# Kernel tuning notes

Measured on AMD Instinct MI355X. Metric: run time of the kernel, lower is better.

## Reference

```python
import jax, jax.numpy as jnp
import numpy as np
from jax import lax

D_STATE = 16
D_CONV = 4
D_MODEL = 1024
D_INNER = 2048
DT_RANK = 64
SEQLEN = 2048
BATCH = 2


def setup_inputs() -> dict:
    key = jax.random.key(0)
    ks = jax.random.split(key, 8)
    hidden_states = jax.random.normal(ks[0], (SEQLEN, BATCH, D_MODEL), jnp.float32)
    W_in = jax.random.normal(ks[1], (2 * D_INNER, D_MODEL), jnp.float32) * (D_MODEL ** -0.5)
    conv_w = jax.random.normal(ks[2], (D_INNER, D_CONV), jnp.float32) * (D_CONV ** -0.5)
    conv_b = jnp.zeros((D_INNER,), jnp.float32)
    W_x = jax.random.normal(ks[3], (DT_RANK + 2 * D_STATE, D_INNER), jnp.float32) * (D_INNER ** -0.5)
    dt_init_std = DT_RANK ** -0.5
    W_dt = jax.random.uniform(ks[4], (D_INNER, DT_RANK), jnp.float32, -dt_init_std, dt_init_std)
    # dt bias init: inverse-softplus of dt ~ LogUniform(1e-3, 1e-1)
    dt = jnp.exp(jax.random.uniform(ks[5], (D_INNER,), jnp.float32) * (np.log(0.1) - np.log(0.001)) + np.log(0.001))
    dt = jnp.clip(dt, 1e-4, None)
    dt_bias = dt + jnp.log(-jnp.expm1(-dt))
    A_log = jnp.log(jnp.tile(jnp.arange(1, D_STATE + 1, dtype=jnp.float32)[None, :], (D_INNER, 1)))
    Dp = jnp.ones((D_INNER,), jnp.float32)
    W_out = jax.random.normal(ks[6], (D_MODEL, D_INNER), jnp.float32) * (D_INNER ** -0.5)
    return {"hidden_states": hidden_states, "W_in": W_in, "conv_w": conv_w, "conv_b": conv_b,
            "W_x": W_x, "W_dt": W_dt, "dt_bias": dt_bias, "A_log": A_log, "D": Dp, "W_out": W_out}


def _mamba_forward(hidden_states, W_in, conv_w, conv_b, W_x, W_dt, dt_bias, A_log, D, W_out):
    L, B, _ = hidden_states.shape
    d_inner, d_state = A_log.shape
    dt_rank = W_dt.shape[1]
    # in_proj: [L,B,D] -> [L,B,2*d_inner] -> [B,2*d_inner,L]
    xz = jnp.einsum('lbd,ed->lbe', hidden_states, W_in)
    xz = jnp.transpose(xz, (1, 2, 0))
    x, z = jnp.split(xz, 2, axis=1)  # each [B,d_inner,L]
    # causal depthwise conv1d + silu
    x = lax.conv_general_dilated(x, conv_w[:, None, :], (1,), [(D_CONV - 1, 0)],
                                 dimension_numbers=('NCH', 'OIH', 'NCH'),
                                 feature_group_count=d_inner)
    x = jax.nn.silu(x + conv_b[None, :, None])  # [B,d_inner,L]
    # x_proj over (b l) tokens
    x_bl = jnp.transpose(x, (0, 2, 1)).reshape(B * L, d_inner)  # (b l) d
    x_dbl = x_bl @ W_x.T  # [(b l), dt_rank + 2*d_state]
    dt_lr, Bm, Cm = jnp.split(x_dbl, [dt_rank, dt_rank + d_state], axis=-1)
    dt = (W_dt @ dt_lr.T).reshape(d_inner, B, L).transpose(1, 0, 2)  # [B,d_inner,L]
    Bm = Bm.reshape(B, L, d_state)  # [B,L,n]
    Cm = Cm.reshape(B, L, d_state)
    # selective scan (delta_softplus=True, delta_bias=dt_bias)
    A = -jnp.exp(A_log)  # [d_inner, n]
    delta = jax.nn.softplus(dt + dt_bias[None, :, None])  # [B,d,L]
    delta_t = jnp.transpose(delta, (2, 0, 1))  # [L,B,d]
    u_t = jnp.transpose(x, (2, 0, 1))          # [L,B,d]
    B_t = jnp.transpose(Bm, (1, 0, 2))         # [L,B,n]
    C_t = jnp.transpose(Cm, (1, 0, 2))         # [L,B,n]

    def step(state, inp):
        d_i, u_i, b_i, c_i = inp
        dA = jnp.exp(d_i[:, :, None] * A[None])           # [B,d,n]
        dBu = (d_i * u_i)[:, :, None] * b_i[:, None, :]   # [B,d,n]
        state = state * dA + dBu
        y = jnp.einsum('bdn,bn->bd', state, c_i)
        return state, y

    init = jnp.zeros((B, d_inner, d_state), delta.dtype)
    _, ys = lax.scan(step, init, (delta_t, u_t, B_t, C_t))  # ys [L,B,d]
    y = jnp.transpose(ys, (1, 0, 2))                         # [B,L,d]
    y = y + jnp.transpose(x, (0, 2, 1)) * D[None, None, :]
    y = y * jax.nn.silu(jnp.transpose(z, (0, 2, 1)))
    out = y @ W_out.T  # [B,L,d_model]
    return jnp.transpose(out, (1, 0, 2))  # [L,B,d_model]


def reference(hidden_states, W_in, conv_w, conv_b, W_x, W_dt, dt_bias, A_log, D, W_out):
    return _mamba_forward(hidden_states, W_in, conv_w, conv_b, W_x, W_dt, dt_bias, A_log, D, W_out)
```

## Files before the change

### kernel.cpp

```cpp
#include <hip/hip_runtime.h>
#include <hip/hip_bf16.h>


#define L_SEQ 2048
#define N_B   2
#define D_M   1024
#define D_I   2048
#define D_ST  16
#define R_DT  64
#define CHNK  32
#define CT    64
#define KS    8
#define DUS   68

using bf16 = __hip_bfloat16;
typedef unsigned short u16;
typedef unsigned int u32;
typedef u16 u16x8 __attribute__((ext_vector_type(8)));
typedef __bf16 bf16x8 __attribute__((ext_vector_type(8)));
typedef float f32x4 __attribute__((ext_vector_type(4)));

__device__ __forceinline__ float b2f(u16 u) {
    union { u32 i; float f; } x;
    x.i = ((u32)u) << 16;
    return x.f;
}
__device__ __forceinline__ u16 f2b(float f) {
    union { bf16 h; u16 s; } x;
    x.h = __float2bfloat16(f);
    return x.s;
}

__device__ __forceinline__ void load4(const float* p, float* o) {
    const float4 v = *(const float4*)p;
    o[0] = v.x; o[1] = v.y; o[2] = v.z; o[3] = v.w;
}
__device__ __forceinline__ void load4(const bf16* p, float* o) {
    const ushort4 v = *(const ushort4*)(const void*)p;
    o[0] = b2f(v.x); o[1] = b2f(v.y); o[2] = b2f(v.z); o[3] = b2f(v.w);
}

__device__ __forceinline__ float softplus_f(float x) {
    return (x > 20.f) ? x : log1pf(__expf(x));
}
__device__ __forceinline__ float silu_f(float x) {
    return x / (1.f + __expf(-x));
}

__device__ __forceinline__ void gl_lds16(const u16* g, u16* l) {
    __builtin_amdgcn_global_load_lds(
        (const __attribute__((address_space(1))) void*)g,
        (__attribute__((address_space(3))) void*)l, 16, 0, 0);
}

template <int EPI>
__global__ __launch_bounds__(256) void bgemm(
    const u16* __restrict__ A, int lda,
    const u16* __restrict__ Wb, int ldb, int K,
    u16* __restrict__ bd, float* __restrict__ fout,
    const float* __restrict__ bias)
{
    __shared__ u16 As[128 * 32];
    __shared__ u16 Bs[64 * 32];

    const int tid = threadIdx.x;
    const int m0 = blockIdx.x * 128;
    const int n0 = blockIdx.y * 64;
    const int w  = tid >> 6;
    const int ln = tid & 63;

    const int sr0 = (w << 4) + (ln >> 2);
    const int sr1 = sr0 + 64;
    const int sx  = ln & 3;
    const int qa0 = (sx - (sr0 >> 1)) & 3;
    const int qa1 = (sx - (sr1 >> 1)) & 3;

    const u16* ga0 = A  + (size_t)(m0 + sr0) * lda + qa0 * 8;
    const u16* ga1 = A  + (size_t)(m0 + sr1) * lda + qa1 * 8;
    const u16* gb0 = Wb + (size_t)(n0 + sr0) * ldb + qa0 * 8;
    u16* la0 = As + ((w << 4) + 0) * 32;
    u16* la1 = As + ((w << 4) + 64) * 32;
    u16* lb0 = Bs + (w << 4) * 32;

    const int wr = (w >> 1) << 6;
    const int wc = (w & 1) << 5;
    const int lm = ln & 15;
    const int qf = ln >> 4;
    int aoff[4], boff[2];
#pragma unroll
    for (int i = 0; i < 4; ++i) {
        const int ra = wr + i * 16 + lm;
        aoff[i] = ra * 32 + (((qf + (ra >> 1)) & 3) << 3);
    }
#pragma unroll
    for (int j = 0; j < 2; ++j) {
        const int rb = wc + j * 16 + lm;
        boff[j] = rb * 32 + (((qf + (rb >> 1)) & 3) << 3);
    }

    f32x4 acc[4][2] = {};

    for (int k0 = 0; k0 < K; k0 += 32) {
        if (k0) __syncthreads();
        gl_lds16(ga0 + k0, la0);
        gl_lds16(ga1 + k0, la1);
        gl_lds16(gb0 + k0, lb0);
        __syncthreads();

        bf16x8 af[4], bfr[2];
#pragma unroll
        for (int i = 0; i < 4; ++i) af[i] = *(const bf16x8*)&As[aoff[i]];
#pragma unroll
        for (int j = 0; j < 2; ++j) bfr[j] = *(const bf16x8*)&Bs[boff[j]];
#pragma unroll
        for (int i = 0; i < 4; ++i)
#pragma unroll
            for (int j = 0; j < 2; ++j)
                acc[i][j] = __builtin_amdgcn_mfma_f32_16x16x32_bf16(
                    af[i], bfr[j], acc[i][j], 0, 0, 0);
    }

    const int qr = (ln >> 4) << 2;
    float bv[2];
    if (EPI == 2) {
#pragma unroll
        for (int j = 0; j < 2; ++j) bv[j] = bias[n0 + wc + j * 16 + lm];
    }
#pragma unroll
    for (int i = 0; i < 4; ++i) {
#pragma unroll
        for (int reg = 0; reg < 4; ++reg) {
            const int rg = m0 + wr + i * 16 + qr + reg;
            if (EPI == 0) {
                const int bb = rg & (N_B - 1);
                const int l = rg >> 1;
                const size_t t = (size_t)bb * L_SEQ + l;
#pragma unroll
                for (int j = 0; j < 2; ++j)
                    bd[t * D_I + n0 + wc + j * 16 + lm] = f2b(acc[i][j][reg]);
            } else if (EPI == 1) {
                const int bb = rg >> 11;
                const int l = rg & (L_SEQ - 1);
                const size_t o = ((size_t)l * N_B + bb) * D_M;
#pragma unroll
                for (int j = 0; j < 2; ++j)
                    fout[o + n0 + wc + j * 16 + lm] = acc[i][j][reg];
            } else if (EPI == 2) {
                const size_t t = (size_t)rg;
#pragma unroll
                for (int j = 0; j < 2; ++j)
                    bd[t * D_I + n0 + wc + j * 16 + lm] =
                        f2b(softplus_f(acc[i][j][reg] + bv[j]));
            } else {
                const int bb = rg & (N_B - 1);
                const int l = rg >> 1;
                const size_t t = (size_t)bb * L_SEQ + l;
#pragma unroll
                for (int j = 0; j < 2; ++j) {
                    u16* p = &bd[t * D_I + n0 + wc + j * 16 + lm];
                    *p = f2b(b2f(*p) * silu_f(acc[i][j][reg]));
                }
            }
        }
    }
}

__global__ __launch_bounds__(256) void xproj_k(
    const u16* __restrict__ u, const u16* __restrict__ Wxb,
    float* __restrict__ Part)
{
    __shared__ u16 As[64 * 32];
    __shared__ u16 Bs[96 * 264];

    const int tid = threadIdx.x;
    const int m0 = blockIdx.x * 64;
    const int kc = blockIdx.y;
    const int kbase = kc * 256;

    for (int e = tid; e < 96 * 32; e += 256) {
        const int row = e >> 5, kq = e & 31;
        const u16x8 v = *(const u16x8*)(Wxb + (size_t)row * D_I + kbase + kq * 8);
        *(u16x8*)&Bs[row * 264 + kq * 8] = v;
    }

    const int w  = tid >> 6;
    const int ln = tid & 63;
    const int sr = (w << 4) + (ln >> 2);
    const int sx = ln & 3;
    const int qa = (sx - (sr >> 1)) & 3;
    const u16* ga = u + (size_t)(m0 + sr) * D_I + kbase + qa * 8;
    u16* la = As + (w << 9);

    const int lm = ln & 15;
    const int qf = ln >> 4;
    const int ra = (w << 4) + lm;
    const int aoff = ra * 32 + (((qf + (ra >> 1)) & 3) << 3);

    f32x4 acc[6] = {};

    for (int it = 0; it < 8; ++it) {
        if (it) __syncthreads();
        gl_lds16(ga + it * 32, la);
        __syncthreads();

        const bf16x8 af = *(const bf16x8*)&As[aoff];
#pragma unroll
        for (int j = 0; j < 6; ++j) {
            const bf16x8 bfv = *(const bf16x8*)&Bs[(j * 16 + lm) * 264 + it * 32 + qf * 8];
            acc[j] = __builtin_amdgcn_mfma_f32_16x16x32_bf16(af, bfv, acc[j], 0, 0, 0);
        }
    }

    const int qr = (ln >> 4) << 2;
#pragma unroll
    for (int j = 0; j < 6; ++j) {
#pragma unroll
        for (int reg = 0; reg < 4; ++reg) {
            const int t = m0 + (w << 4) + qr + reg;
            Part[((size_t)kc * (N_B * L_SEQ) + t) * 96 + j * 16 + lm] = acc[j][reg];
        }
    }
}

__global__ __launch_bounds__(256) void xreduce(
    const float* __restrict__ Part, u16* __restrict__ dtlr,
    float* __restrict__ Bm, float* __restrict__ Cm)
{
    const int e = blockIdx.x * 256 + threadIdx.x;
    const int t = e / 96, c = e - t * 96;
    float s = 0.f;
#pragma unroll
    for (int kc = 0; kc < KS; ++kc)
        s += Part[(size_t)kc * (N_B * L_SEQ * 96) + e];
    if (c < 64)      dtlr[t * 64 + c] = f2b(s);
    else if (c < 80) Bm[t * 16 + (c - 64)] = s;
    else             Cm[t * 16 + (c - 80)] = s;
}

__global__ __launch_bounds__(256) void cvt_k(const float* __restrict__ s,
                                             u16* __restrict__ d)
{
    const size_t i = ((size_t)blockIdx.x * 256 + threadIdx.x) * 8;
    const float4 a = *(const float4*)(s + i);
    const float4 b = *(const float4*)(s + i + 4);
    u16 t[8] = {f2b(a.x), f2b(a.y), f2b(a.z), f2b(a.w),
                f2b(b.x), f2b(b.y), f2b(b.z), f2b(b.w)};
    *(u16x8*)(d + i) = *(const u16x8*)t;
}

__global__ __launch_bounds__(256) void conv_k(
    const bf16* __restrict__ x, const float* __restrict__ cw,
    const float* __restrict__ cb, bf16* __restrict__ xc)
{
    const int t = blockIdx.x;
    const int l = t & (L_SEQ - 1);
#pragma unroll
    for (int it = 0; it < 2; ++it) {
        const int d = ((int)threadIdx.x + it * 256) << 2;
        float w[4][4], bias[4], acc[4];
#pragma unroll
        for (int dd = 0; dd < 4; ++dd)
            load4(cw + (size_t)(d + dd) * 4, w[dd]);
        load4(cb + d, bias);
#pragma unroll
        for (int dd = 0; dd < 4; ++dd) acc[dd] = bias[dd];
#pragma unroll
        for (int j = 0; j < 4; ++j) {
            const int ll = l - 3 + j;
            if (ll >= 0) {
                float xv[4];
                load4(x + (size_t)(t - 3 + j) * D_I + d, xv);
#pragma unroll
                for (int dd = 0; dd < 4; ++dd)
                    acc[dd] = fmaf(xv[dd], w[dd][j], acc[dd]);
            }
        }
        const ushort4 v = make_ushort4(f2b(silu_f(acc[0])), f2b(silu_f(acc[1])),
                                       f2b(silu_f(acc[2])), f2b(silu_f(acc[3])));
        *(ushort4*)(void*)(xc + (size_t)t * D_I + d) = v;
    }
}

template <int PHASE>
__global__ __launch_bounds__(256) void scan_chunk(
    bf16* __restrict__ dy, const bf16* __restrict__ u,
    const float* __restrict__ Bm, const float* __restrict__ Cm,
    const float* __restrict__ Alog, const float* __restrict__ Dp,
    float* __restrict__ Pc, float* __restrict__ Qc,
    const float* __restrict__ Sin)
{
    __shared__ u32 duS[(CT / 2) * DUS];
    __shared__ float Bs[CT][D_ST];
    __shared__ float Cs[(PHASE == 1) ? CT : 1][D_ST];

    const int tid = threadIdx.x;
    const int d0 = blockIdx.x * 64;
    const int b  = blockIdx.y;
    const int c  = blockIdx.z;
    const int row0 = b * L_SEQ + c * CT;

    const int sl = tid >> 3;
    const int sg = tid & 7;

    u32 wB[8];
    {
        const size_t goA = (size_t)(row0 + sl) * D_I + d0 + sg * 8;
        const size_t goB = goA + (size_t)(CT / 2) * D_I;
        const u16x8 dA8 = *(const u16x8*)((const u16*)dy + goA);
        const u16x8 uA8 = *(const u16x8*)((const u16*)u + goA);
        const u16x8 dB8 = *(const u16x8*)((const u16*)dy + goB);
        const u16x8 uB8 = *(const u16x8*)((const u16*)u + goB);
        u32 wA[8];
#pragma unroll
        for (int j = 0; j < 8; ++j) {
            wA[j] = (u32)dA8[j] | ((u32)uA8[j] << 16);
            wB[j] = (u32)dB8[j] | ((u32)uB8[j] << 16);
        }
        *(uint4*)&duS[sl * DUS + sg * 8]     = make_uint4(wA[0], wA[1], wA[2], wA[3]);
        *(uint4*)&duS[sl * DUS + sg * 8 + 4] = make_uint4(wA[4], wA[5], wA[6], wA[7]);
    }
    {
        const float4* src = (const float4*)(Bm + (size_t)row0 * D_ST);
        float4* dst = (float4*)Bs;
        for (int e = tid; e < CT * D_ST / 4; e += 256) dst[e] = src[e];
        if (PHASE == 1) {
            const float4* s2 = (const float4*)(Cm + (size_t)row0 * D_ST);
            float4* d2 = (float4*)Cs;
            for (int e = tid; e < CT * D_ST / 4; e += 256) d2[e] = s2[e];
        }
    }
    __syncthreads();

    const int dl = tid >> 2;
    const int d  = d0 + dl;
    const int ns = tid & 3;
    const size_t pqbase = (((size_t)b * CHNK + c) * D_I + d) * D_ST + ns * 4;

    float Av[4];
    {
        const float4 a4 = *(const float4*)(Alog + (size_t)d * D_ST + ns * 4);
        const float l2e = 1.4426950408889634f;
        Av[0] = -__expf(a4.x) * l2e; Av[1] = -__expf(a4.y) * l2e;
        Av[2] = -__expf(a4.z) * l2e; Av[3] = -__expf(a4.w) * l2e;
    }

    float st[4] = {0.f, 0.f, 0.f, 0.f};
    float sdv = 0.f;
    if (PHASE == 1) {
        const float4 s0 = *(const float4*)(Sin + pqbase);
        st[0] = s0.x; st[1] = s0.y; st[2] = s0.z; st[3] = s0.w;
    }
    const float Dd = (PHASE == 1) ? Dp[d] : 0.f;

#pragma unroll
    for (int half = 0; half < 2; ++half) {
        if (half) {
            __syncthreads();
            if (PHASE == 1) {
                u16 t[8];
#pragma unroll
                for (int j = 0; j < 8; ++j)
                    t[j] = (u16)(duS[sl * DUS + sg * 8 + j] & 0xFFFFu);
                *(u16x8*)((u16*)dy + (size_t)(row0 + sl) * D_I + d0 + sg * 8) =
                    *(const u16x8*)t;
                __syncthreads();
            }
            *(uint4*)&duS[sl * DUS + sg * 8]     = make_uint4(wB[0], wB[1], wB[2], wB[3]);
            *(uint4*)&duS[sl * DUS + sg * 8 + 4] = make_uint4(wB[4], wB[5], wB[6], wB[7]);
            __syncthreads();
        }
        const int lb = half * (CT / 2);
#pragma unroll 2
        for (int l = 0; l < CT / 2; ++l) {
            const u32 w0 = duS[l * DUS + dl];
            union { u32 i; float f; } dvv, uvv;
            dvv.i = w0 << 16;
            uvv.i = w0 & 0xFFFF0000u;
            const float dv = dvv.f, uv = uvv.f;
            const float dvu = dv * uv;

            float bn[4], cn[4] = {0.f, 0.f, 0.f, 0.f};
            {
                const float4 b4 = *(const float4*)&Bs[lb + l][ns * 4];
                bn[0] = b4.x; bn[1] = b4.y; bn[2] = b4.z; bn[3] = b4.w;
            }
            if (PHASE == 1) {
                const float4 c4 = *(const float4*)&Cs[lb + l][ns * 4];
                cn[0] = c4.x; cn[1] = c4.y; cn[2] = c4.z; cn[3] = c4.w;
            }
            if (PHASE == 0) sdv += dv;

            float y = 0.f;
#pragma unroll
            for (int j = 0; j < 4; ++j) {
                const float dA = __builtin_amdgcn_exp2f(dv * Av[j]);
                st[j] = fmaf(st[j], dA, dvu * bn[j]);
                if (PHASE == 1) y = fmaf(st[j], cn[j], y);
            }
            if (PHASE == 1) {
                y += __shfl_xor(y, 1);
                y += __shfl_xor(y, 2);
                if (ns == 0)
                    ((u16*)duS)[(l * DUS + dl) * 2] = f2b(y + uv * Dd);
            }
        }
    }

    if (PHASE == 0) {
        *(float4*)(Pc + pqbase) = make_float4(
            __builtin_amdgcn_exp2f(sdv * Av[0]), __builtin_amdgcn_exp2f(sdv * Av[1]),
            __builtin_amdgcn_exp2f(sdv * Av[2]), __builtin_amdgcn_exp2f(sdv * Av[3]));
        *(float4*)(Qc + pqbase) = make_float4(st[0], st[1], st[2], st[3]);
    } else {
        __syncthreads();
        u16 t[8];
#pragma unroll
        for (int j = 0; j < 8; ++j)
            t[j] = (u16)(duS[sl * DUS + sg * 8 + j] & 0xFFFFu);
        *(u16x8*)((u16*)dy + (size_t)(row0 + CT / 2 + sl) * D_I + d0 + sg * 8) =
            *(const u16x8*)t;
    }
}

__global__ __launch_bounds__(256) void scan_comb(
    const float* Pc, const float* Qc, float* Sin)
{
    const int b = blockIdx.y;
    const int d = blockIdx.x * 16 + (threadIdx.x >> 4);
    const int n = threadIdx.x & 15;
    const size_t i0 = (((size_t)b * CHNK) * D_I + d) * D_ST + n;
    const size_t cs = (size_t)D_I * D_ST;

    float p[CHNK], q[CHNK];
#pragma unroll
    for (int c = 0; c < CHNK; ++c) {
        p[c] = Pc[i0 + c * cs];
        q[c] = Qc[i0 + c * cs];
    }
    float s = 0.f;
#pragma unroll
    for (int c = 0; c < CHNK; ++c) {
        Sin[i0 + c * cs] = s;
        s = fmaf(s, p[c], q[c]);
    }
}

__global__ void zfill(float* o) {
    o[(size_t)blockIdx.x * 256 + threadIdx.x] = 0.f;
}

extern "C" void kernel_launch(void* const* d_in, const int* in_sizes, int n_in,
                              void* d_out, int out_size, void* d_ws, size_t ws_size,
                              hipStream_t stream)
{
    const float* hs   = (const float*)d_in[0];
    const float* Win  = (const float*)d_in[1];
    const float* cw   = (const float*)d_in[2];
    const float* cb   = (const float*)d_in[3];
    const float* Wx   = (const float*)d_in[4];
    const float* Wdt  = (const float*)d_in[5];
    const float* dtb  = (const float*)d_in[6];
    const float* Alog = (const float*)d_in[7];
    const float* Dp   = (const float*)d_in[8];
    const float* Wout = (const float*)d_in[9];
    float* out = (float*)d_out;

    const size_t SZ = (size_t)N_B * L_SEQ * D_I;
    const size_t NT = (size_t)N_B * L_SEQ;
    const size_t NHS   = NT * D_M;
    const size_t NWIN  = (size_t)2 * D_I * D_M;
    const size_t NWOUT = (size_t)D_M * D_I;
    const size_t NWX   = (size_t)96 * D_I;
    const size_t NWDT  = (size_t)D_I * R_DT;
    const size_t NEED = SZ * 2 * sizeof(bf16)
                      + (NHS + NWIN + NWOUT + NWX + NWDT + NT * R_DT) * sizeof(u16)
                      + NT * 2 * D_ST * sizeof(float);
    if (ws_size < NEED) {
        zfill<<<dim3((unsigned)((size_t)out_size / 256)), 256, 0, stream>>>(out);
        return;
    }

    bf16* RA   = (bf16*)d_ws;
    bf16* RB   = RA + SZ;
    u16* bhs   = (u16*)(RB + SZ);
    u16* bWin  = bhs + NHS;
    u16* bWout = bWin + NWIN;
    u16* bWx   = bWout + NWOUT;
    u16* bWdt  = bWx + NWX;
    u16* dtlr  = bWdt + NWDT;
    float* Bm  = (float*)(dtlr + NT * R_DT);
    float* Cm  = Bm + NT * D_ST;
    float* Part = out;
    const size_t PQ = (size_t)N_B * CHNK * D_I * D_ST;
    float* Pc  = out;
    float* Qc  = Pc + PQ;
    float* Sin = Pc;

    cvt_k<<<dim3((unsigned)(NHS / 2048)), 256, 0, stream>>>(hs, bhs);
    cvt_k<<<dim3((unsigned)(NWIN / 2048)), 256, 0, stream>>>(Win, bWin);
    cvt_k<<<dim3((unsigned)(NWOUT / 2048)), 256, 0, stream>>>(Wout, bWout);
    cvt_k<<<dim3((unsigned)(NWX / 2048)), 256, 0, stream>>>(Wx, bWx);
    cvt_k<<<dim3((unsigned)(NWDT / 2048)), 256, 0, stream>>>(Wdt, bWdt);
    bgemm<0><<<dim3(32, 32), 256, 0, stream>>>(
        bhs, D_M, bWin, D_M, D_M, (u16*)RA, nullptr, nullptr);
    conv_k<<<dim3(N_B * L_SEQ), 256, 0, stream>>>(RA, cw, cb, RB);
    xproj_k<<<dim3(64, KS), 256, 0, stream>>>((const u16*)RB, bWx, Part);
    xreduce<<<dim3((unsigned)(NT * 96 / 256)), 256, 0, stream>>>(Part, dtlr, Bm, Cm);
    bgemm<2><<<dim3(32, 32), 256, 0, stream>>>(
        dtlr, R_DT, bWdt, R_DT, R_DT, (u16*)RA, nullptr, dtb);
    scan_chunk<0><<<dim3(D_I / 64, N_B, CHNK), 256, 0, stream>>>(
        RA, RB, Bm, Cm, Alog, Dp, Pc, Qc, nullptr);
    scan_comb<<<dim3(D_I / 16, N_B), 256, 0, stream>>>(Pc, Qc, Sin);
    scan_chunk<1><<<dim3(D_I / 64, N_B, CHNK), 256, 0, stream>>>(
        RA, RB, Bm, Cm, Alog, Dp, nullptr, nullptr, Sin);
    bgemm<3><<<dim3(32, 32), 256, 0, stream>>>(
        bhs, D_M, bWin + (size_t)D_I * D_M, D_M, D_M, (u16*)RA, nullptr, nullptr);
    bgemm<1><<<dim3(32, 16), 256, 0, stream>>>(
        (const u16*)RA, D_I, bWout, D_I, D_I, nullptr, out, nullptr);
}
```

Before: 348.4 us.

## Fuse dt projection into scan chunks and merge weight conversion kernels

Removes the separate dt-projection GEMM: each scan_chunk block now computes delta for its 64x64 tile with MFMA from the low-rank dt vector and W_dt, applies softplus, and writes it straight into shared memory. This avoids writing and rereading the full delta tensor through global memory. The cost is that delta is computed twice, once in each scan phase. The five fp32-to-bf16 conversion launches are merged into one kernel, and the shared-memory tile moves from padding to an XOR swizzle to avoid bank conflicts.

Result: slower. 361.2 us (+3.7%).

```diff
diff --git a/kernel.cpp b/kernel.cpp
--- a/kernel.cpp
+++ b/kernel.cpp
@@ -11,7 +11,6 @@
 #define CHNK  32
 #define CT    64
 #define KS    8
-#define DUS   68
 
 using bf16 = __hip_bfloat16;
 typedef unsigned short u16;
@@ -121,11 +120,6 @@
     }
 
     const int qr = (ln >> 4) << 2;
-    float bv[2];
-    if (EPI == 2) {
-#pragma unroll
-        for (int j = 0; j < 2; ++j) bv[j] = bias[n0 + wc + j * 16 + lm];
-    }
 #pragma unroll
     for (int i = 0; i < 4; ++i) {
 #pragma unroll
@@ -145,12 +139,6 @@
 #pragma unroll
                 for (int j = 0; j < 2; ++j)
                     fout[o + n0 + wc + j * 16 + lm] = acc[i][j][reg];
-            } else if (EPI == 2) {
-                const size_t t = (size_t)rg;
-#pragma unroll
-                for (int j = 0; j < 2; ++j)
-                    bd[t * D_I + n0 + wc + j * 16 + lm] =
-                        f2b(softplus_f(acc[i][j][reg] + bv[j]));
             } else {
                 const int bb = rg & (N_B - 1);
                 const int l = rg >> 1;
@@ -237,10 +225,21 @@
     else             Cm[t * 16 + (c - 80)] = s;
 }
 
-__global__ __launch_bounds__(256) void cvt_k(const float* __restrict__ s,
-                                             u16* __restrict__ d)
-{
-    const size_t i = ((size_t)blockIdx.x * 256 + threadIdx.x) * 8;
+__global__ __launch_bounds__(256) void cvt_all(
+    const float* __restrict__ s0, u16* __restrict__ d0,
+    const float* __restrict__ s1, u16* __restrict__ d1,
+    const float* __restrict__ s2, u16* __restrict__ d2,
+    const float* __restrict__ s3, u16* __restrict__ d3,
+    const float* __restrict__ s4, u16* __restrict__ d4)
+{
+    const int bid = blockIdx.x;
+    const float* s; u16* d; size_t off;
+    if (bid < 2048)      { s = s0; d = d0; off = (size_t)bid * 2048; }
+    else if (bid < 4096) { s = s1; d = d1; off = (size_t)(bid - 2048) * 2048; }
+    else if (bid < 5120) { s = s2; d = d2; off = (size_t)(bid - 4096) * 2048; }
+    else if (bid < 5216) { s = s3; d = d3; off = (size_t)(bid - 5120) * 2048; }
+    else                 { s = s4; d = d4; off = (size_t)(bid - 5216) * 2048; }
+    const size_t i = off + (size_t)threadIdx.x * 8;
     const float4 a = *(const float4*)(s + i);
     const float4 b = *(const float4*)(s + i + 4);
     u16 t[8] = {f2b(a.x), f2b(a.y), f2b(a.z), f2b(a.w),
@@ -287,9 +286,12 @@
     const float* __restrict__ Bm, const float* __restrict__ Cm,
     const float* __restrict__ Alog, const float* __restrict__ Dp,
     float* __restrict__ Pc, float* __restrict__ Qc,
-    const float* __restrict__ Sin)
-{
-    __shared__ u32 duS[(CT / 2) * DUS];
+    const float* __restrict__ Sin,
+    const u16* __restrict__ dtlr, const u16* __restrict__ Wdt,
+    const float* __restrict__ dtb)
+{
+    __shared__ u32 duS[32 * 64];
+    __shared__ u16 dBS[32 * 64];
     __shared__ float Bs[CT][D_ST];
     __shared__ float Cs[(PHASE == 1) ? CT : 1][D_ST];
 
@@ -299,25 +301,37 @@
     const int c  = blockIdx.z;
     const int row0 = b * L_SEQ + c * CT;
 
+    const int w  = tid >> 6;
+    const int ln = tid & 63;
+    const int lm = ln & 15;
+    const int qf = ln >> 4;
+
+    const bf16x8 af0 = *(const bf16x8*)(
+        dtlr + (size_t)(row0 + (w << 4) + lm) * R_DT + qf * 8);
+    bf16x8 bf0[4];
+#pragma unroll
+    for (int j = 0; j < 4; ++j)
+        bf0[j] = *(const bf16x8*)(
+            Wdt + (size_t)(d0 + j * 16 + lm) * R_DT + qf * 8);
+
     const int sl = tid >> 3;
     const int sg = tid & 7;
-
-    u32 wB[8];
+    const int c0 = (sg * 8) ^ ((sl & 3) << 3);
+
+    u16 uB16[8];
     {
         const size_t goA = (size_t)(row0 + sl) * D_I + d0 + sg * 8;
-        const size_t goB = goA + (size_t)(CT / 2) * D_I;
-        const u16x8 dA8 = *(const u16x8*)((const u16*)dy + goA);
+        const size_t goB = goA + (size_t)32 * D_I;
         const u16x8 uA8 = *(const u16x8*)((const u16*)u + goA);
-        const u16x8 dB8 = *(const u16x8*)((const u16*)dy + goB);
         const u16x8 uB8 = *(const u16x8*)((const u16*)u + goB);
         u32 wA[8];
 #pragma unroll
         for (int j = 0; j < 8; ++j) {
-            wA[j] = (u32)dA8[j] | ((u32)uA8[j] << 16);
-            wB[j] = (u32)dB8[j] | ((u32)uB8[j] << 16);
-        }
-        *(uint4*)&duS[sl * DUS + sg * 8]     = make_uint4(wA[0], wA[1], wA[2], wA[3]);
-        *(uint4*)&duS[sl * DUS + sg * 8 + 4] = make_uint4(wA[4], wA[5], wA[6], wA[7]);
+            wA[j] = ((u32)uA8[j]) << 16;
+            uB16[j] = uB8[j];
+        }
+        *(uint4*)&duS[sl * 64 + c0]     = make_uint4(wA[0], wA[1], wA[2], wA[3]);
+        *(uint4*)&duS[sl * 64 + c0 + 4] = make_uint4(wA[4], wA[5], wA[6], wA[7]);
     }
     {
         const float4* src = (const float4*)(Bm + (size_t)row0 * D_ST);
@@ -331,6 +345,39 @@
     }
     __syncthreads();
 
+    {
+        f32x4 dac[4] = {};
+#pragma unroll
+        for (int j = 0; j < 4; ++j)
+            dac[j] = __builtin_amdgcn_mfma_f32_16x16x32_bf16(
+                af0, bf0[j], dac[j], 0, 0, 0);
+        const bf16x8 af1 = *(const bf16x8*)(
+            dtlr + (size_t)(row0 + (w << 4) + lm) * R_DT + 32 + qf * 8);
+#pragma unroll
+        for (int j = 0; j < 4; ++j) {
+            const bf16x8 bf1 = *(const bf16x8*)(
+                Wdt + (size_t)(d0 + j * 16 + lm) * R_DT + 32 + qf * 8);
+            dac[j] = __builtin_amdgcn_mfma_f32_16x16x32_bf16(
+                af1, bf1, dac[j], 0, 0, 0);
+        }
+#pragma unroll
+        for (int j = 0; j < 4; ++j) {
+            const float bv = dtb[d0 + j * 16 + lm];
+            const int dd = j * 16 + lm;
+#pragma unroll
+            for (int reg = 0; reg < 4; ++reg) {
+                const int l = (w << 4) + (qf << 2) + reg;
+                const u16 dv16 = f2b(softplus_f(dac[j][reg] + bv));
+                const int sw = (l & 3) << 3;
+                if (l < 32)
+                    ((u16*)duS)[(l * 64 + (dd ^ sw)) * 2] = dv16;
+                else
+                    dBS[(l - 32) * 64 + (dd ^ sw)] = dv16;
+            }
+        }
+    }
+    __syncthreads();
+
     const int dl = tid >> 2;
     const int d  = d0 + dl;
     const int ns = tid & 3;
@@ -360,19 +407,25 @@
                 u16 t[8];
 #pragma unroll
                 for (int j = 0; j < 8; ++j)
-                    t[j] = (u16)(duS[sl * DUS + sg * 8 + j] & 0xFFFFu);
+                    t[j] = (u16)(duS[sl * 64 + c0 + j] & 0xFFFFu);
                 *(u16x8*)((u16*)dy + (size_t)(row0 + sl) * D_I + d0 + sg * 8) =
                     *(const u16x8*)t;
                 __syncthreads();
             }
-            *(uint4*)&duS[sl * DUS + sg * 8]     = make_uint4(wB[0], wB[1], wB[2], wB[3]);
-            *(uint4*)&duS[sl * DUS + sg * 8 + 4] = make_uint4(wB[4], wB[5], wB[6], wB[7]);
+            const u16x8 d8 = *(const u16x8*)&dBS[sl * 64 + c0];
+            u32 wB[8];
+#pragma unroll
+            for (int j = 0; j < 8; ++j)
+                wB[j] = (u32)d8[j] | ((u32)uB16[j] << 16);
+            *(uint4*)&duS[sl * 64 + c0]     = make_uint4(wB[0], wB[1], wB[2], wB[3]);
+            *(uint4*)&duS[sl * 64 + c0 + 4] = make_uint4(wB[4], wB[5], wB[6], wB[7]);
             __syncthreads();
         }
-        const int lb = half * (CT / 2);
+        const int lb = half * 32;
 #pragma unroll 2
-        for (int l = 0; l < CT / 2; ++l) {
-            const u32 w0 = duS[l * DUS + dl];
+        for (int l = 0; l < 32; ++l) {
+            const int sw = (l & 3) << 3;
+            const u32 w0 = duS[l * 64 + (dl ^ sw)];
             union { u32 i; float f; } dvv, uvv;
             dvv.i = w0 << 16;
             uvv.i = w0 & 0xFFFF0000u;
@@ -401,7 +454,7 @@
                 y += __shfl_xor(y, 1);
                 y += __shfl_xor(y, 2);
                 if (ns == 0)
-                    ((u16*)duS)[(l * DUS + dl) * 2] = f2b(y + uv * Dd);
+                    ((u16*)duS)[(l * 64 + (dl ^ sw)) * 2] = f2b(y + uv * Dd);
             }
         }
     }
@@ -416,8 +469,8 @@
         u16 t[8];
 #pragma unroll
         for (int j = 0; j < 8; ++j)
-            t[j] = (u16)(duS[sl * DUS + sg * 8 + j] & 0xFFFFu);
-        *(u16x8*)((u16*)dy + (size_t)(row0 + CT / 2 + sl) * D_I + d0 + sg * 8) =
+            t[j] = (u16)(duS[sl * 64 + c0 + j] & 0xFFFFu);
+        *(u16x8*)((u16*)dy + (size_t)(row0 + 32 + sl) * D_I + d0 + sg * 8) =
             *(const u16x8*)t;
     }
 }
@@ -496,23 +549,18 @@
     float* Qc  = Pc + PQ;
     float* Sin = Pc;
 
-    cvt_k<<<dim3((unsigned)(NHS / 2048)), 256, 0, stream>>>(hs, bhs);
-    cvt_k<<<dim3((unsigned)(NWIN / 2048)), 256, 0, stream>>>(Win, bWin);
-    cvt_k<<<dim3((unsigned)(NWOUT / 2048)), 256, 0, stream>>>(Wout, bWout);
-    cvt_k<<<dim3((unsigned)(NWX / 2048)), 256, 0, stream>>>(Wx, bWx);
-    cvt_k<<<dim3((unsigned)(NWDT / 2048)), 256, 0, stream>>>(Wdt, bWdt);
+    cvt_all<<<dim3(5280), 256, 0, stream>>>(
+        hs, bhs, Win, bWin, Wout, bWout, Wx, bWx, Wdt, bWdt);
     bgemm<0><<<dim3(32, 32), 256, 0, stream>>>(
         bhs, D_M, bWin, D_M, D_M, (u16*)RA, nullptr, nullptr);
     conv_k<<<dim3(N_B * L_SEQ), 256, 0, stream>>>(RA, cw, cb, RB);
     xproj_k<<<dim3(64, KS), 256, 0, stream>>>((const u16*)RB, bWx, Part);
     xreduce<<<dim3((unsigned)(NT * 96 / 256)), 256, 0, stream>>>(Part, dtlr, Bm, Cm);
-    bgemm<2><<<dim3(32, 32), 256, 0, stream>>>(
-        dtlr, R_DT, bWdt, R_DT, R_DT, (u16*)RA, nullptr, dtb);
     scan_chunk<0><<<dim3(D_I / 64, N_B, CHNK), 256, 0, stream>>>(
-        RA, RB, Bm, Cm, Alog, Dp, Pc, Qc, nullptr);
+        RA, RB, Bm, Cm, Alog, Dp, Pc, Qc, nullptr, dtlr, bWdt, dtb);
     scan_comb<<<dim3(D_I / 16, N_B), 256, 0, stream>>>(Pc, Qc, Sin);
     scan_chunk<1><<<dim3(D_I / 64, N_B, CHNK), 256, 0, stream>>>(
-        RA, RB, Bm, Cm, Alog, Dp, nullptr, nullptr, Sin);
+        RA, RB, Bm, Cm, Alog, Dp, nullptr, nullptr, Sin, dtlr, bWdt, dtb);
     bgemm<3><<<dim3(32, 32), 256, 0, stream>>>(
         bhs, D_M, bWin + (size_t)D_I * D_M, D_M, D_M, (u16*)RA, nullptr, nullptr);
     bgemm<1><<<dim3(32, 16), 256, 0, stream>>>(
```
